# Kernel optimization log

Hardware: AMD Instinct MI355X
Metric: run time of the kernel (lower is better)

Reference implementation:

```python
import jax, jax.numpy as jnp
import numpy as np

RADIUS = 0.15
NSAMPLE = 128
NPOINT = 128
EPS = 1e-5  # BatchNorm eps (eval mode, running_mean=0, running_var=1)


def _bn(x, g, b):
    shape = (1, -1) + (1,) * (x.ndim - 2)
    return x * (g / jnp.sqrt(1.0 + EPS)).reshape(shape) + b.reshape(shape)


def _fps(x, npoint):
    # farthest point sampling; x: (Bk, N, 3) -> (Bk, npoint) int32
    Bn, N, _ = x.shape

    def step(carry, _):
        dist, far = carry
        c = jnp.take_along_axis(x, far[:, None, None], 1)  # (Bk,1,3)
        d = jnp.sum((x - c) ** 2, -1)
        dist = jnp.minimum(dist, d)
        return (dist, jnp.argmax(dist, -1).astype(jnp.int32)), far

    init = (jnp.full((Bn, N), 1e10, x.dtype), jnp.zeros((Bn,), jnp.int32))
    _, idxs = jax.lax.scan(step, init, None, length=npoint)
    return idxs.T  # (Bk, npoint)


def _sa_module(x, f, mlp):
    # PointnetSAModuleVotes: FPS -> ball query -> group (use_xyz, normalize_xyz)
    # -> shared MLP (conv2d 1x1 + BN + ReLU) -> max over nsample.
    Bk, M, _ = x.shape
    fps_idx = _fps(x, NPOINT)
    new_xyz = jnp.take_along_axis(x, fps_idx[..., None], 1)  # (Bk,np,3)
    d2 = jnp.sum((new_xyz[:, :, None, :] - x[:, None, :, :]) ** 2, -1)  # (Bk,np,M)
    cand = jnp.where(d2 < RADIUS ** 2, jnp.arange(M)[None, None, :], M)
    cand = jnp.sort(cand, -1)[..., :NSAMPLE]  # first nsample in-radius indices
    first = cand[..., :1]
    first = jnp.where(first == M, 0, first)
    idx = jnp.where(cand == M, first, cand)  # (Bk,np,ns), pad with first valid
    gx = jnp.take_along_axis(x, idx.reshape(Bk, -1)[..., None], 1).reshape(Bk, NPOINT, NSAMPLE, 3)
    gxn = (gx - new_xyz[:, :, None, :]) / RADIUS  # normalize_xyz=True
    gf = jnp.take_along_axis(f[:, :, None, :], idx[:, None, :, :], 3)  # (Bk,C,np,ns)
    h = jnp.concatenate([gxn.transpose(0, 3, 1, 2), gf], 1)  # (Bk, C+3, np, ns)
    for (w, b, g, be) in mlp:
        h = jax.nn.relu(_bn(jnp.einsum('oc,bcps->bops', w, h) + b[None, :, None, None], g, be))
    return new_xyz, h.max(-1)  # (Bk,np,3), (Bk,128,np)


def setup_inputs() -> dict:
    key = jax.random.key(0)
    ks = iter(jax.random.split(key, 40))
    B, M, K, C = 2, 1024, 19, 256
    inp = {}
    inp['xyz'] = jax.random.normal(next(ks), (B, M, K, 3), jnp.float32)
    inp['features'] = jax.random.normal(next(ks), (B, C, K, M), jnp.float32)

    def conv_p(prefix, cin, cout):
        inp[prefix + '_w'] = jax.random.normal(next(ks), (cout, cin), jnp.float32) * (1.0 / np.sqrt(cin))
        inp[prefix + '_b'] = jax.random.normal(next(ks), (cout,), jnp.float32) * 0.02
        inp[prefix + '_g'] = 1.0 + 0.1 * jax.random.normal(next(ks), (cout,), jnp.float32)
        inp[prefix + '_be'] = 0.02 * jax.random.normal(next(ks), (cout,), jnp.float32)

    conv_p('m1', C + 3, 128)  # use_xyz -> 259 in-channels
    conv_p('m2', 128, 128)
    conv_p('m3', 128, 128)
    conv_p('c1', 128, 128)
    conv_p('c2', 128, 128)
    inp['op_w'] = jax.random.normal(next(ks), (K, 5, 128), jnp.float32) * (1.0 / np.sqrt(128))
    inp['op_b'] = jax.random.normal(next(ks), (K, 5), jnp.float32) * 0.02
    return inp


def reference(xyz, features, m1_w, m1_b, m1_g, m1_be, m2_w, m2_b, m2_g, m2_be,
              m3_w, m3_b, m3_g, m3_be, c1_w, c1_b, c1_g, c1_be,
              c2_w, c2_b, c2_g, c2_be, op_w, op_b):
    B, M, K, _ = xyz.shape
    C = features.shape[1]
    # fold vote_factor k into the batch dim (all per-k SA/conv weights are shared)
    x = xyz.transpose(0, 2, 1, 3).reshape(B * K, M, 3)
    f = features.transpose(0, 2, 1, 3).reshape(B * K, C, M)
    mlp = [(m1_w, m1_b, m1_g, m1_be), (m2_w, m2_b, m2_g, m2_be), (m3_w, m3_b, m3_g, m3_be)]
    new_xyz, feat = _sa_module(x, f, mlp)
    net = jax.nn.relu(_bn(jnp.einsum('oc,bcp->bop', c1_w, feat) + c1_b[None, :, None], c1_g, c1_be))
    net = jax.nn.relu(_bn(jnp.einsum('oc,bcp->bop', c2_w, net) + c2_b[None, :, None], c2_g, c2_be))
    net = net.reshape(B, K, 128, NPOINT)
    # per-k output conv (conv_op ModuleList), 128 -> 2+3
    out = jnp.einsum('koc,bkcp->bkop', op_w, net) + op_b[None, :, :, None]
    net_t = out.transpose(0, 1, 3, 2)  # (B,K,np,5)
    agg_xyz = new_xyz.reshape(B, K, NPOINT, 3)
    center = agg_xyz + net_t[..., 2:5]  # decode_scores_
    scores = jnp.concatenate([net_t[..., :2], center], -1)  # obj(2) + center(3)
    return scores, agg_xyz, feat.reshape(B, K, 128, NPOINT)
```

## Files before the change

kernel.cpp:

```cpp
#include <hip/hip_runtime.h>
#include <math.h>

#define NBK   38

#define OFF_XC    0u
#define OFF_NXYZ  466944u
#define OFF_BIDX  525312u
#define OFF_W1F   3015680u
#define OFF_PREP  22938624u
#define OFF_WT    22955008u
#define OFF_WF    23086080u
#define OFF_CNT   23348224u

#define OUT_AGG   24320
#define OUT_FEAT  38912

typedef short bf16x8 __attribute__((ext_vector_type(8)));
typedef float f32x4  __attribute__((ext_vector_type(4)));
typedef int   v4i    __attribute__((ext_vector_type(4)));
typedef int   v2i    __attribute__((ext_vector_type(2)));

__device__ __forceinline__ float dist2f(float a0, float a1, float a2,
                                        float b0, float b1, float b2) {
#pragma clang fp contract(off)
  float d0 = a0 - b0;
  float d1 = a1 - b1;
  float d2 = a2 - b2;
  return d0 * d0 + d1 * d1 + d2 * d2;
}

__device__ __forceinline__ void split2rn(float v, unsigned& sh, unsigned& sm) {
  unsigned u = __float_as_uint(v);
  unsigned rh = (u + 0x7fffu + ((u >> 16) & 1u)) & 0xffff0000u;
  sh = rh >> 16;
  float r1 = v - __uint_as_float(rh);
  unsigned u1 = __float_as_uint(r1);
  unsigned rm = (u1 + 0x7fffu + ((u1 >> 16) & 1u)) & 0xffff0000u;
  sm = rm >> 16;
}

__global__ __launch_bounds__(256) void prep_kernel(
    const float* __restrict__ m1w, const float* __restrict__ m1g, const float* __restrict__ m1be,
    const float* __restrict__ m2b, const float* __restrict__ m2g, const float* __restrict__ m2be,
    const float* __restrict__ m3b, const float* __restrict__ m3g, const float* __restrict__ m3be,
    const float* __restrict__ c1b, const float* __restrict__ c1g, const float* __restrict__ c1be,
    const float* __restrict__ c2b, const float* __restrict__ c2g, const float* __restrict__ c2be,
    float* __restrict__ prep)
{
  int t = threadIdx.x;
  if (t < 128) {
    float inv = 1.0f / sqrtf(1.0f + 1e-5f);
    float a1 = m1g[t] * inv;
    prep[t] = a1;
    float a2 = m2g[t] * inv;  prep[256 + t] = a2;  prep[384 + t] = fmaf(m2b[t], a2, m2be[t]);
    float a3 = m3g[t] * inv;  prep[512 + t] = a3;  prep[640 + t] = fmaf(m3b[t], a3, m3be[t]);
    float ac1 = c1g[t] * inv; prep[768 + t] = ac1; prep[896 + t] = fmaf(c1b[t], ac1, c1be[t]);
    float ac2 = c2g[t] * inv; prep[1024 + t] = ac2; prep[1152 + t] = fmaf(c2b[t], ac2, c2be[t]);
    prep[1280 + 4 * t + 0] = m1w[t * 259 + 0] * a1;
    prep[1280 + 4 * t + 1] = m1w[t * 259 + 1] * a1;
    prep[1280 + 4 * t + 2] = m1w[t * 259 + 2] * a1;
    prep[1280 + 4 * t + 3] = m1be[t];
  }
}

__global__ __launch_bounds__(256) void wsplit_kernel(
    const float* __restrict__ m1w, const float* __restrict__ m2w,
    const float* __restrict__ m3w, const float* __restrict__ c1w,
    const float* __restrict__ c2w, short* __restrict__ Wf, float* __restrict__ wt)
{
  int idx = blockIdx.x * 256 + threadIdx.x;
#pragma unroll
  for (int e = 0; e < 4; ++e) {
    int i = idx * 4 + e;
    if (i < 32768) {
      int c = i & 127, o = (i >> 7) & 127, l = i >> 14;
      float w = (l ? m3w : m2w)[o * 128 + c];
      unsigned sh, sm;
      split2rn(w, sh, sm);
      int ot = o >> 4, mm = o & 15, kk = c >> 5, q = (c & 31) >> 3, j = c & 7;
      int within = (q * 16 + mm) * 8 + j;
      Wf[(((l * 2 + 0) * 4 + kk) * 8 + ot) * 512 + within] = (short)sh;
      Wf[(((l * 2 + 1) * 4 + kk) * 8 + ot) * 512 + within] = (short)sm;
    } else {
      int jdx = i - 32768;
      int o = jdx >> 8, c = jdx & 255;
      float w = m1w[o * 259 + 3 + c];
      unsigned sh, sm;
      split2rn(w, sh, sm);
      int ot = o >> 4, mm = o & 15, kk = c >> 5, q = (c & 31) >> 3, j = c & 7;
      int within = (q * 16 + mm) * 8 + j;
      Wf[65536 + ((kk) * 8 + ot) * 512 + within] = (short)sh;
      Wf[65536 + ((8 + kk) * 8 + ot) * 512 + within] = (short)sm;
    }
  }
  {
    int i = idx;
    int c = i >> 7, o = i & 127;
    wt[i] = c1w[o * 128 + c];
    wt[16384 + i] = c2w[o * 128 + c];
  }
}

__global__ __launch_bounds__(256) void fps_kernel(const float* __restrict__ xyz,
    float* __restrict__ xc, float* __restrict__ nxyz, float* __restrict__ agg)
{
  int bk = blockIdx.x, t = threadIdx.x;
  int b = bk / 19, k = bk % 19;
  int wave = t >> 6, lane = t & 63;
  __shared__ float sx0[1024], sx1[1024], sx2[1024];
  __shared__ unsigned long long skey[8];
  float x0[4], x1[4], x2[4], dist[4];
#pragma unroll
  for (int j = 0; j < 4; ++j) {
    int i = j * 256 + t;
    const float* src = xyz + ((size_t)((b * 1024 + i) * 19 + k)) * 3;
    x0[j] = src[0]; x1[j] = src[1]; x2[j] = src[2];
    sx0[i] = x0[j]; sx1[i] = x1[j]; sx2[i] = x2[j];
    xc[(bk * 3 + 0) * 1024 + i] = x0[j];
    xc[(bk * 3 + 1) * 1024 + i] = x1[j];
    xc[(bk * 3 + 2) * 1024 + i] = x2[j];
    dist[j] = 1e10f;
  }
  int far = 0;
  __syncthreads();
  for (int it = 0; it < 128; ++it) {
    float c0 = sx0[far], c1 = sx1[far], c2 = sx2[far];
    if (t < 3) {
      float cv = (t == 0) ? c0 : ((t == 1) ? c1 : c2);
      nxyz[(bk * 128 + it) * 3 + t] = cv;
      agg[(bk * 128 + it) * 3 + t]  = cv;
    }
    unsigned long long best = 0ull;
#pragma unroll
    for (int j = 0; j < 4; ++j) {
      int i = j * 256 + t;
      float d = dist2f(x0[j], x1[j], x2[j], c0, c1, c2);
      float dj = fminf(dist[j], d);
      dist[j] = dj;
      unsigned long long key =
          ((unsigned long long)__float_as_uint(dj) << 32) | (unsigned)(1023 - i);
      if (key > best) best = key;
    }
#pragma unroll
    for (int off = 32; off > 0; off >>= 1) {
      unsigned hi = (unsigned)(best >> 32), lo = (unsigned)best;
      unsigned h2 = __shfl_xor(hi, off);
      unsigned l2 = __shfl_xor(lo, off);
      unsigned long long ob = ((unsigned long long)h2 << 32) | l2;
      if (ob > best) best = ob;
    }
    if (lane == 0) skey[(it & 1) * 4 + wave] = best;
    __syncthreads();
    unsigned long long bb = skey[(it & 1) * 4 + (lane & 3)];
#pragma unroll
    for (int off = 1; off <= 2; off <<= 1) {
      unsigned hi = (unsigned)(bb >> 32), lo = (unsigned)bb;
      unsigned h2 = __shfl_xor(hi, off);
      unsigned l2 = __shfl_xor(lo, off);
      unsigned long long ob = ((unsigned long long)h2 << 32) | l2;
      if (ob > bb) bb = ob;
    }
    far = 1023 - (int)(bb & 0xffffffffu);
  }
}

__global__ __launch_bounds__(64) void ball_kernel(const float* __restrict__ xc,
    const float* __restrict__ nxyz, int* __restrict__ bidx, int* __restrict__ counts)
{
  int gb = blockIdx.x;
  int bk = gb >> 7, p = gb & 127, lane = threadIdx.x;
  const float* x0 = xc + (bk * 3 + 0) * 1024;
  const float* x1 = xc + (bk * 3 + 1) * 1024;
  const float* x2 = xc + (bk * 3 + 2) * 1024;
  float c0 = nxyz[(bk * 128 + p) * 3 + 0];
  float c1 = nxyz[(bk * 128 + p) * 3 + 1];
  float c2 = nxyz[(bk * 128 + p) * 3 + 2];
  int* out = bidx + ((size_t)gb) * 128;
  int count = 0, first = 0;
  bool got = false;
  for (int ch = 0; ch < 16 && count < 128; ++ch) {
    int m = (ch << 6) + lane;
    float d = dist2f(x0[m], x1[m], x2[m], c0, c1, c2);
    bool flag = d < 0.0225f;
    unsigned long long mask = __ballot(flag);
    if (!got && mask) { first = (ch << 6) + __builtin_ctzll(mask); got = true; }
    int pos = count + (int)__popcll(mask & ((1ull << lane) - 1ull));
    if (flag && pos < 128) out[pos] = m;
    count += (int)__popcll(mask);
  }
  for (int j = count + lane; j < 128; j += 64) out[j] = first;
  if (lane == 0) counts[gb] = count > 128 ? 128 : count;
}

__global__ __launch_bounds__(256, 2) void w1f_kernel(
    const float* __restrict__ feats, const float* __restrict__ m1b,
    const float* __restrict__ prep, const short* __restrict__ Wf,
    float* __restrict__ W1f)
{
  __shared__ __align__(16) short ffrag[16384];
  int blk = blockIdx.x;
  int bk = blk >> 3, m0 = (blk & 7) << 7;
  int b = bk / 19, k = bk % 19;
  int t = threadIdx.x;
  int wave = t >> 6, lane = t & 63;
  int quad = lane >> 4, nl = lane & 15;
  int mloc = t & 127, chalf = t >> 7;
  int st_w = mloc >> 4, sl_w = mloc & 15;
  const float* fbase = feats + ((size_t)(b * 4864 + k)) * 1024 + m0 + mloc;
  const short* WA = Wf + 65536;

  f32x4 acc[2][8];
#pragma unroll
  for (int oi = 0; oi < 2; ++oi)
#pragma unroll
    for (int st = 0; st < 8; ++st) acc[oi][st] = (f32x4){0.f, 0.f, 0.f, 0.f};

  for (int ch = 0; ch < 4; ++ch) {
    int cbase = ch * 64 + chalf * 32;
#pragma unroll
    for (int g = 0; g < 4; ++g) {
      float v[8];
#pragma unroll
      for (int j = 0; j < 8; ++j)
        v[j] = fbase[(size_t)(cbase + g * 8 + j) * 19456];
      unsigned sh[8], sm[8];
#pragma unroll
      for (int j = 0; j < 8; ++j) split2rn(v[j], sh[j], sm[j]);
      int base = chalf * 4096 + st_w * 512 + (g * 16 + sl_w) * 8;
      v4i ph = {(int)(sh[0] | (sh[1] << 16)), (int)(sh[2] | (sh[3] << 16)),
                (int)(sh[4] | (sh[5] << 16)), (int)(sh[6] | (sh[7] << 16))};
      *(v4i*)&ffrag[base] = ph;
      v4i pm = {(int)(sm[0] | (sm[1] << 16)), (int)(sm[2] | (sm[3] << 16)),
                (int)(sm[4] | (sm[5] << 16)), (int)(sm[6] | (sm[7] << 16))};
      *(v4i*)&ffrag[base + 8192] = pm;
    }
    __syncthreads();
#pragma unroll
    for (int kkl = 0; kkl < 2; ++kkl) {
      int kk = ch * 2 + kkl;
      bf16x8 a[2][2];
#pragma unroll
      for (int oi = 0; oi < 2; ++oi)
#pragma unroll
        for (int sp = 0; sp < 2; ++sp)
          a[oi][sp] = *(const bf16x8*)(WA + ((sp * 8 + kk) * 8 + wave * 2 + oi) * 512 + lane * 8);
#pragma unroll
      for (int st = 0; st < 8; ++st) {
        const short* hb = ffrag + kkl * 4096 + st * 512 + lane * 8;
        bf16x8 b0 = *(const bf16x8*)hb;
        bf16x8 b1 = *(const bf16x8*)(hb + 8192);
#pragma unroll
        for (int oi = 0; oi < 2; ++oi) {
          f32x4 c = acc[oi][st];
          c = __builtin_amdgcn_mfma_f32_16x16x32_bf16(a[oi][1], b0, c, 0, 0, 0);
          c = __builtin_amdgcn_mfma_f32_16x16x32_bf16(a[oi][0], b1, c, 0, 0, 0);
          c = __builtin_amdgcn_mfma_f32_16x16x32_bf16(a[oi][0], b0, c, 0, 0, 0);
          acc[oi][st] = c;
        }
      }
    }
    __syncthreads();
  }
#pragma unroll
  for (int oi = 0; oi < 2; ++oi) {
    int o0 = (wave * 2 + oi) * 16 + quad * 4;
    float4 bb = *(const float4*)&m1b[o0];
    float4 al = *(const float4*)&prep[o0];
#pragma unroll
    for (int st = 0; st < 8; ++st) {
      int m_out = m0 + st * 16 + nl;
      f32x4 cc = acc[oi][st];
      float4 r;
      r.x = (cc[0] + bb.x) * al.x;
      r.y = (cc[1] + bb.y) * al.y;
      r.z = (cc[2] + bb.z) * al.z;
      r.w = (cc[3] + bb.w) * al.w;
      *(float4*)&W1f[((size_t)(bk * 1024 + m_out)) * 128 + o0] = r;
    }
  }
}

__device__ __forceinline__ void mfma_layer(const short* __restrict__ Wf,
                                           const short* hfrag, int l,
                                           int wave, int lane, int nst_h,
                                           f32x4 acc[2][4])
{
#pragma unroll 1
  for (int kk = 0; kk < 4; ++kk) {
    bf16x8 a[2][2];
#pragma unroll
    for (int oi = 0; oi < 2; ++oi)
#pragma unroll
      for (int sp = 0; sp < 2; ++sp)
        a[oi][sp] = *(const bf16x8*)(Wf + (((l * 2 + sp) * 4 + kk) * 8 + (wave * 2 + oi)) * 512 + lane * 8);
    for (int st = 0; st < nst_h; ++st) {
      const short* hb = hfrag + kk * 2048 + st * 512 + lane * 8;
      bf16x8 b0 = *(const bf16x8*)(hb);
      bf16x8 b1 = *(const bf16x8*)(hb + 8192);
#pragma unroll
      for (int oi = 0; oi < 2; ++oi) {
        f32x4 c = acc[oi][st];
        c = __builtin_amdgcn_mfma_f32_16x16x32_bf16(a[oi][1], b0, c, 0, 0, 0);
        c = __builtin_amdgcn_mfma_f32_16x16x32_bf16(a[oi][0], b1, c, 0, 0, 0);
        c = __builtin_amdgcn_mfma_f32_16x16x32_bf16(a[oi][0], b0, c, 0, 0, 0);
        acc[oi][st] = c;
      }
    }
  }
}

__global__ __launch_bounds__(256, 4) void sa_kernel(
    const float* __restrict__ xc, const float* __restrict__ nxyz,
    const int* __restrict__ bidx, const int* __restrict__ counts,
    const float* __restrict__ W1f, const float* __restrict__ prep,
    const short* __restrict__ Wf, float* __restrict__ feat_out)
{
  __shared__ __align__(16) short hfrag[16384];
  __shared__ float pcs[512];
  int gb = blockIdx.x, bk = gb >> 7, p = gb & 127;
  int t = threadIdx.x;
  int wave = t >> 6, lane = t & 63;
  int quad = lane >> 4, nl = lane & 15;

  pcs[t] = prep[1280 + t];
  pcs[256 + t] = prep[1536 + t];

  int scount = counts[gb];
  int nst = (scount + 15) >> 4;

  float cen0 = nxyz[(bk * 128 + p) * 3 + 0];
  float cen1 = nxyz[(bk * 128 + p) * 3 + 1];
  float cen2 = nxyz[(bk * 128 + p) * 3 + 2];

  float rmax[2][4] = {{0.f, 0.f, 0.f, 0.f}, {0.f, 0.f, 0.f, 0.f}};
  __syncthreads();

  for (int hh = 0; hh < 2; ++hh) {
    int nst_h = nst - hh * 4;
    if (nst_h <= 0) break;
    if (nst_h > 4) nst_h = 4;
    {
      int cg = wave;
      int st = lane >> 4, sl = lane & 15;
      if (st < nst_h) {
        int m = bidx[((size_t)gb) * 128 + hh * 64 + lane];
        float g0 = (xc[(bk * 3 + 0) * 1024 + m] - cen0) * (1.0f / 0.15f);
        float g1 = (xc[(bk * 3 + 1) * 1024 + m] - cen1) * (1.0f / 0.15f);
        float g2 = (xc[(bk * 3 + 2) * 1024 + m] - cen2) * (1.0f / 0.15f);
        const float4* wrow = (const float4*)(W1f + ((size_t)(bk * 1024 + m)) * 128 + cg * 32);
        const float4* pcp = (const float4*)pcs + cg * 32;
#pragma unroll
        for (int g = 0; g < 4; ++g) {
          float4 wva = wrow[g * 2], wvb = wrow[g * 2 + 1];
          float wv[8] = {wva.x, wva.y, wva.z, wva.w, wvb.x, wvb.y, wvb.z, wvb.w};
          unsigned sh[8], sm[8];
#pragma unroll
          for (int e = 0; e < 8; ++e) {
            float4 pc = pcp[g * 8 + e];
            float hv = fmaxf(wv[e] + pc.x * g0 + pc.y * g1 + pc.z * g2 + pc.w, 0.f);
            split2rn(hv, sh[e], sm[e]);
          }
          int base = (cg * 4 + st) * 512 + (g * 16 + sl) * 8;
          v4i ph = {(int)(sh[0] | (sh[1] << 16)), (int)(sh[2] | (sh[3] << 16)),
                    (int)(sh[4] | (sh[5] << 16)), (int)(sh[6] | (sh[7] << 16))};
          *(v4i*)&hfrag[base] = ph;
          v4i pm = {(int)(sm[0] | (sm[1] << 16)), (int)(sm[2] | (sm[3] << 16)),
                    (int)(sm[4] | (sm[5] << 16)), (int)(sm[6] | (sm[7] << 16))};
          *(v4i*)&hfrag[base + 8192] = pm;
        }
      }
    }
    __syncthreads();

    f32x4 acc[2][4];
#pragma unroll
    for (int oi = 0; oi < 2; ++oi)
#pragma unroll
      for (int st = 0; st < 4; ++st) acc[oi][st] = (f32x4){0.f, 0.f, 0.f, 0.f};
    mfma_layer(Wf, hfrag, 0, wave, lane, nst_h, acc);
    __syncthreads();

#pragma unroll
    for (int oi = 0; oi < 2; ++oi) {
      int o0 = (wave * 2 + oi) * 16 + quad * 4;
      float4 al = *(const float4*)&prep[256 + o0];
      float4 be = *(const float4*)&prep[384 + o0];
      int kk2 = o0 >> 5, g2 = (o0 & 31) >> 3, j0 = o0 & 7;
      for (int st = 0; st < nst_h; ++st) {
        f32x4 cc = acc[oi][st];
        float v0 = fmaxf(fmaf(cc[0], al.x, be.x), 0.f);
        float v1 = fmaxf(fmaf(cc[1], al.y, be.y), 0.f);
        float v2 = fmaxf(fmaf(cc[2], al.z, be.z), 0.f);
        float v3 = fmaxf(fmaf(cc[3], al.w, be.w), 0.f);
        unsigned h0, m0_, h1, m1_, h2, m2_, h3, m3_;
        split2rn(v0, h0, m0_); split2rn(v1, h1, m1_);
        split2rn(v2, h2, m2_); split2rn(v3, h3, m3_);
        int base = (kk2 * 4 + st) * 512 + (g2 * 16 + nl) * 8 + j0;
        v2i w0 = {(int)(h0 | (h1 << 16)), (int)(h2 | (h3 << 16))};
        *(v2i*)&hfrag[base] = w0;
        v2i w1 = {(int)(m0_ | (m1_ << 16)), (int)(m2_ | (m3_ << 16))};
        *(v2i*)&hfrag[base + 8192] = w1;
      }
    }
    __syncthreads();

#pragma unroll
    for (int oi = 0; oi < 2; ++oi)
#pragma unroll
      for (int st = 0; st < 4; ++st) acc[oi][st] = (f32x4){0.f, 0.f, 0.f, 0.f};
    mfma_layer(Wf, hfrag, 1, wave, lane, nst_h, acc);

#pragma unroll
    for (int oi = 0; oi < 2; ++oi) {
      int o0 = (wave * 2 + oi) * 16 + quad * 4;
      float4 al = *(const float4*)&prep[512 + o0];
      float4 be = *(const float4*)&prep[640 + o0];
      for (int st = 0; st < nst_h; ++st) {
        f32x4 cc = acc[oi][st];
        rmax[oi][0] = fmaxf(rmax[oi][0], fmaxf(fmaf(cc[0], al.x, be.x), 0.f));
        rmax[oi][1] = fmaxf(rmax[oi][1], fmaxf(fmaf(cc[1], al.y, be.y), 0.f));
        rmax[oi][2] = fmaxf(rmax[oi][2], fmaxf(fmaf(cc[2], al.z, be.z), 0.f));
        rmax[oi][3] = fmaxf(rmax[oi][3], fmaxf(fmaf(cc[3], al.w, be.w), 0.f));
      }
    }
    __syncthreads();
  }

#pragma unroll
  for (int oi = 0; oi < 2; ++oi)
#pragma unroll
    for (int r = 0; r < 4; ++r) {
      float v = rmax[oi][r];
      v = fmaxf(v, __shfl_xor(v, 1));
      v = fmaxf(v, __shfl_xor(v, 2));
      v = fmaxf(v, __shfl_xor(v, 4));
      v = fmaxf(v, __shfl_xor(v, 8));
      if (nl == 0) {
        int o = (wave * 2 + oi) * 16 + quad * 4 + r;
        feat_out[(((size_t)bk) << 14) + (o << 7) + p] = v;
      }
    }
}

__device__ __forceinline__ void gemm_tile(const float* __restrict__ w,
                                          const float* lds, int tx, int ty,
                                          float acc[8][8])
{
#pragma unroll
  for (int i = 0; i < 8; ++i)
#pragma unroll
    for (int j = 0; j < 8; ++j) acc[i][j] = 0.f;
  for (int c = 0; c < 128; ++c) {
    const float4* wr = (const float4*)(w + c * 128 + ty * 8);
    float4 a0 = wr[0], a1 = wr[1];
    const float4* hr = (const float4*)(lds + c * 128 + tx * 8);
    float4 b0 = hr[0], b1 = hr[1];
    float av[8] = {a0.x, a0.y, a0.z, a0.w, a1.x, a1.y, a1.z, a1.w};
    float bv[8] = {b0.x, b0.y, b0.z, b0.w, b1.x, b1.y, b1.z, b1.w};
#pragma unroll
    for (int i = 0; i < 8; ++i)
#pragma unroll
      for (int j = 0; j < 8; ++j) acc[i][j] = fmaf(av[i], bv[j], acc[i][j]);
  }
}

__global__ __launch_bounds__(256) void head_kernel(const float* __restrict__ featg,
    const float* __restrict__ prep, const float* __restrict__ wt,
    const float* __restrict__ nxyz, const float* __restrict__ opw,
    const float* __restrict__ opb, float* __restrict__ scores)
{
  __shared__ __align__(16) float buf[128 * 128];
  int bk = blockIdx.x, t = threadIdx.x;
  for (int i = t; i < 16384; i += 256) buf[i] = featg[(bk << 14) + i];
  __syncthreads();
  int tx = t & 15, ty = t >> 4;
  float acc[8][8];

  gemm_tile(wt, buf, tx, ty, acc);
  __syncthreads();
#pragma unroll
  for (int i = 0; i < 8; ++i) {
    int o = ty * 8 + i;
    float al = prep[768 + o], be = prep[896 + o];
#pragma unroll
    for (int j = 0; j < 8; ++j)
      buf[o * 128 + tx * 8 + j] = fmaxf(fmaf(acc[i][j], al, be), 0.f);
  }
  __syncthreads();

  gemm_tile(wt + 16384, buf, tx, ty, acc);
  __syncthreads();
#pragma unroll
  for (int i = 0; i < 8; ++i) {
    int o = ty * 8 + i;
    float al = prep[1024 + o], be = prep[1152 + o];
#pragma unroll
    for (int j = 0; j < 8; ++j)
      buf[o * 128 + tx * 8 + j] = fmaxf(fmaf(acc[i][j], al, be), 0.f);
  }
  __syncthreads();

  if (t < 128) {
    int p = t, k = bk % 19;
    float res[5];
#pragma unroll
    for (int j = 0; j < 5; ++j) {
      const float* wr = opw + ((size_t)(k * 5 + j)) * 128;
      float a = opb[k * 5 + j];
      for (int c = 0; c < 128; ++c) a = fmaf(wr[c], buf[c * 128 + p], a);
      res[j] = a;
    }
    float a0 = nxyz[(bk * 128 + p) * 3 + 0];
    float a1 = nxyz[(bk * 128 + p) * 3 + 1];
    float a2 = nxyz[(bk * 128 + p) * 3 + 2];
    float* sc = scores + ((size_t)(bk * 128 + p)) * 5;
    sc[0] = res[0];
    sc[1] = res[1];
    sc[2] = a0 + res[2];
    sc[3] = a1 + res[3];
    sc[4] = a2 + res[4];
  }
}

extern "C" void kernel_launch(void* const* d_in, const int* in_sizes, int n_in,
                              void* d_out, int out_size, void* d_ws, size_t ws_size,
                              hipStream_t stream) {
  (void)in_sizes; (void)n_in; (void)out_size; (void)ws_size;
  const float* xyz  = (const float*)d_in[0];
  const float* fts  = (const float*)d_in[1];
  const float* m1w  = (const float*)d_in[2];
  const float* m1b  = (const float*)d_in[3];
  const float* m1g  = (const float*)d_in[4];
  const float* m1be = (const float*)d_in[5];
  const float* m2w  = (const float*)d_in[6];
  const float* m2b  = (const float*)d_in[7];
  const float* m2g  = (const float*)d_in[8];
  const float* m2be = (const float*)d_in[9];
  const float* m3w  = (const float*)d_in[10];
  const float* m3b  = (const float*)d_in[11];
  const float* m3g  = (const float*)d_in[12];
  const float* m3be = (const float*)d_in[13];
  const float* c1w  = (const float*)d_in[14];
  const float* c1b  = (const float*)d_in[15];
  const float* c1g  = (const float*)d_in[16];
  const float* c1be = (const float*)d_in[17];
  const float* c2w  = (const float*)d_in[18];
  const float* c2b  = (const float*)d_in[19];
  const float* c2g  = (const float*)d_in[20];
  const float* c2be = (const float*)d_in[21];
  const float* opw  = (const float*)d_in[22];
  const float* opb  = (const float*)d_in[23];

  float* out = (float*)d_out;
  char* ws = (char*)d_ws;
  float* xc   = (float*)(ws + OFF_XC);
  float* nxyz = (float*)(ws + OFF_NXYZ);
  int*   bidx = (int*)(ws + OFF_BIDX);
  float* W1f  = (float*)(ws + OFF_W1F);
  float* prep = (float*)(ws + OFF_PREP);
  float* wt   = (float*)(ws + OFF_WT);
  short* Wf   = (short*)(ws + OFF_WF);
  int*   cnt  = (int*)(ws + OFF_CNT);

  hipLaunchKernelGGL(prep_kernel, dim3(1), dim3(256), 0, stream,
                     m1w, m1g, m1be, m2b, m2g, m2be, m3b, m3g, m3be,
                     c1b, c1g, c1be, c2b, c2g, c2be, prep);
  hipLaunchKernelGGL(wsplit_kernel, dim3(64), dim3(256), 0, stream,
                     m1w, m2w, m3w, c1w, c2w, Wf, wt);
  hipLaunchKernelGGL(fps_kernel, dim3(NBK), dim3(256), 0, stream,
                     xyz, xc, nxyz, out + OUT_AGG);
  hipLaunchKernelGGL(ball_kernel, dim3(NBK * 128), dim3(64), 0, stream,
                     xc, nxyz, bidx, cnt);
  hipLaunchKernelGGL(w1f_kernel, dim3(NBK * 8), dim3(256), 0, stream,
                     fts, m1b, prep, Wf, W1f);
  hipLaunchKernelGGL(sa_kernel, dim3(NBK * 128), dim3(256), 0, stream,
                     xc, nxyz, bidx, cnt, W1f, prep, Wf, out + OUT_FEAT);
  hipLaunchKernelGGL(head_kernel, dim3(NBK), dim3(256), 0, stream,
                     out + OUT_FEAT, prep, wt, nxyz, opw, opb, out);
}
```

Measured before the change: 342.3 us.

## Pack four centroids' sample tiles per SA block and simplify FPS argmax

The SA kernel now processes four sampled centroids per block. It concatenates their 16-sample tiles into a shared stream, so partially filled tiles no longer waste MFMA work and block count drops fourfold. Per-tile max results go to shared memory and are reduced per centroid at the end. FPS replaces the 64-bit key shuffle reduction with a float max reduction plus ballot, and carries the winner's coordinates through shared memory instead of indexing a shared point copy. The costs are extra shared memory, a lower occupancy hint, and fewer blocks, which may underfill the GPU.

```diff
diff --git a/kernel.cpp b/kernel.cpp
--- a/kernel.cpp
+++ b/kernel.cpp
@@ -107,60 +107,82 @@
   int bk = blockIdx.x, t = threadIdx.x;
   int b = bk / 19, k = bk % 19;
   int wave = t >> 6, lane = t & 63;
-  __shared__ float sx0[1024], sx1[1024], sx2[1024];
-  __shared__ unsigned long long skey[8];
+  __shared__ int scand[2][4][8];
   float x0[4], x1[4], x2[4], dist[4];
 #pragma unroll
   for (int j = 0; j < 4; ++j) {
     int i = j * 256 + t;
     const float* src = xyz + ((size_t)((b * 1024 + i) * 19 + k)) * 3;
     x0[j] = src[0]; x1[j] = src[1]; x2[j] = src[2];
-    sx0[i] = x0[j]; sx1[i] = x1[j]; sx2[i] = x2[j];
     xc[(bk * 3 + 0) * 1024 + i] = x0[j];
     xc[(bk * 3 + 1) * 1024 + i] = x1[j];
     xc[(bk * 3 + 2) * 1024 + i] = x2[j];
     dist[j] = 1e10f;
   }
-  int far = 0;
-  __syncthreads();
+  if (t == 0) {
+#pragma unroll
+    for (int w = 0; w < 4; ++w) {
+      scand[0][w][0] = 0;
+      scand[0][w][1] = 1023;
+      scand[0][w][2] = __float_as_int(x0[0]);
+      scand[0][w][3] = __float_as_int(x1[0]);
+      scand[0][w][4] = __float_as_int(x2[0]);
+    }
+  }
+  __syncthreads();
+
   for (int it = 0; it < 128; ++it) {
-    float c0 = sx0[far], c1 = sx1[far], c2 = sx2[far];
+    int pi = it & 1;
+    v4i s0 = *(const v4i*)&scand[pi][0][0]; int z0 = scand[pi][0][4];
+    v4i s1 = *(const v4i*)&scand[pi][1][0]; int z1 = scand[pi][1][4];
+    v4i s2 = *(const v4i*)&scand[pi][2][0]; int z2 = scand[pi][2][4];
+    v4i s3 = *(const v4i*)&scand[pi][3][0]; int z3 = scand[pi][3][4];
+    unsigned long long k0 = ((unsigned long long)(unsigned)s0.x << 32) | (unsigned)s0.y;
+    unsigned long long k1 = ((unsigned long long)(unsigned)s1.x << 32) | (unsigned)s1.y;
+    unsigned long long k2 = ((unsigned long long)(unsigned)s2.x << 32) | (unsigned)s2.y;
+    unsigned long long k3 = ((unsigned long long)(unsigned)s3.x << 32) | (unsigned)s3.y;
+    if (k1 > k0) { k0 = k1; s0 = s1; z0 = z1; }
+    if (k3 > k2) { k2 = k3; s2 = s3; z2 = z3; }
+    if (k2 > k0) { k0 = k2; s0 = s2; z0 = z2; }
+    float c0 = __int_as_float(s0.z);
+    float c1 = __int_as_float(s0.w);
+    float c2 = __int_as_float(z0);
     if (t < 3) {
       float cv = (t == 0) ? c0 : ((t == 1) ? c1 : c2);
       nxyz[(bk * 128 + it) * 3 + t] = cv;
       agg[(bk * 128 + it) * 3 + t]  = cv;
     }
-    unsigned long long best = 0ull;
 #pragma unroll
     for (int j = 0; j < 4; ++j) {
-      int i = j * 256 + t;
       float d = dist2f(x0[j], x1[j], x2[j], c0, c1, c2);
-      float dj = fminf(dist[j], d);
-      dist[j] = dj;
-      unsigned long long key =
-          ((unsigned long long)__float_as_uint(dj) << 32) | (unsigned)(1023 - i);
-      if (key > best) best = key;
-    }
-#pragma unroll
-    for (int off = 32; off > 0; off >>= 1) {
-      unsigned hi = (unsigned)(best >> 32), lo = (unsigned)best;
-      unsigned h2 = __shfl_xor(hi, off);
-      unsigned l2 = __shfl_xor(lo, off);
-      unsigned long long ob = ((unsigned long long)h2 << 32) | l2;
-      if (ob > best) best = ob;
-    }
-    if (lane == 0) skey[(it & 1) * 4 + wave] = best;
+      dist[j] = fminf(dist[j], d);
+    }
+    float dmax = fmaxf(fmaxf(dist[0], dist[1]), fmaxf(dist[2], dist[3]));
+#pragma unroll
+    for (int off = 1; off <= 32; off <<= 1)
+      dmax = fmaxf(dmax, __shfl_xor(dmax, off));
+    unsigned long long b0 = __ballot(dist[0] == dmax);
+    unsigned long long b1 = __ballot(dist[1] == dmax);
+    unsigned long long b2 = __ballot(dist[2] == dmax);
+    unsigned long long b3 = __ballot(dist[3] == dmax);
+    int idx;
+    if (b0)      idx =       (wave << 6) + __builtin_ctzll(b0);
+    else if (b1) idx = 256 + (wave << 6) + __builtin_ctzll(b1);
+    else if (b2) idx = 512 + (wave << 6) + __builtin_ctzll(b2);
+    else         idx = 768 + (wave << 6) + __builtin_ctzll(b3);
+    if (lane == (idx & 63)) {
+      int j = idx >> 8;
+      float w0 = (j == 0) ? x0[0] : (j == 1) ? x0[1] : (j == 2) ? x0[2] : x0[3];
+      float w1 = (j == 0) ? x1[0] : (j == 1) ? x1[1] : (j == 2) ? x1[2] : x1[3];
+      float w2 = (j == 0) ? x2[0] : (j == 1) ? x2[1] : (j == 2) ? x2[2] : x2[3];
+      int* slot = &scand[pi ^ 1][wave][0];
+      slot[0] = __float_as_int(dmax);
+      slot[1] = 1023 - idx;
+      slot[2] = __float_as_int(w0);
+      slot[3] = __float_as_int(w1);
+      slot[4] = __float_as_int(w2);
+    }
     __syncthreads();
-    unsigned long long bb = skey[(it & 1) * 4 + (lane & 3)];
-#pragma unroll
-    for (int off = 1; off <= 2; off <<= 1) {
-      unsigned hi = (unsigned)(bb >> 32), lo = (unsigned)bb;
-      unsigned h2 = __shfl_xor(hi, off);
-      unsigned l2 = __shfl_xor(lo, off);
-      unsigned long long ob = ((unsigned long long)h2 << 32) | l2;
-      if (ob > bb) bb = ob;
-    }
-    far = 1023 - (int)(bb & 0xffffffffu);
   }
 }
 
@@ -309,7 +331,7 @@
   }
 }
 
-__global__ __launch_bounds__(256, 4) void sa_kernel(
+__global__ __launch_bounds__(256, 3) void sa_kernel(
     const float* __restrict__ xc, const float* __restrict__ nxyz,
     const int* __restrict__ bidx, const int* __restrict__ counts,
     const float* __restrict__ W1f, const float* __restrict__ prep,
@@ -317,33 +339,41 @@
 {
   __shared__ __align__(16) short hfrag[16384];
   __shared__ float pcs[512];
-  int gb = blockIdx.x, bk = gb >> 7, p = gb & 127;
+  __shared__ float sm[32 * 128];
+  __shared__ float ccen[12];
+  __shared__ int scnt[4];
+  int gb = blockIdx.x, bk = gb >> 5, pb = (gb & 31) << 2;
   int t = threadIdx.x;
   int wave = t >> 6, lane = t & 63;
   int quad = lane >> 4, nl = lane & 15;
 
   pcs[t] = prep[1280 + t];
   pcs[256 + t] = prep[1536 + t];
-
-  int scount = counts[gb];
-  int nst = (scount + 15) >> 4;
-
-  float cen0 = nxyz[(bk * 128 + p) * 3 + 0];
-  float cen1 = nxyz[(bk * 128 + p) * 3 + 1];
-  float cen2 = nxyz[(bk * 128 + p) * 3 + 2];
-
-  float rmax[2][4] = {{0.f, 0.f, 0.f, 0.f}, {0.f, 0.f, 0.f, 0.f}};
-  __syncthreads();
-
-  for (int hh = 0; hh < 2; ++hh) {
-    int nst_h = nst - hh * 4;
-    if (nst_h <= 0) break;
+  if (t < 4) scnt[t] = counts[bk * 128 + pb + t];
+  if (t < 12) ccen[t] = nxyz[(bk * 128 + pb + (t >> 2) % 4) * 3 + 0];
+  __syncthreads();
+  if (t < 12) {
+    int bb = t / 3, c = t % 3;
+    ccen[t] = nxyz[(bk * 128 + pb + bb) * 3 + c];
+  }
+  int n0 = (scnt[0] + 15) >> 4, n1 = (scnt[1] + 15) >> 4;
+  int n2 = (scnt[2] + 15) >> 4, n3 = (scnt[3] + 15) >> 4;
+  int pf1 = n0, pf2 = n0 + n1, pf3 = n0 + n1 + n2, T = n0 + n1 + n2 + n3;
+  __syncthreads();
+
+  for (int q0 = 0; q0 < T; q0 += 4) {
+    int nst_h = T - q0;
     if (nst_h > 4) nst_h = 4;
     {
       int cg = wave;
       int st = lane >> 4, sl = lane & 15;
       if (st < nst_h) {
-        int m = bidx[((size_t)gb) * 128 + hh * 64 + lane];
+        int q = q0 + st;
+        int bq = (q >= pf1) + (q >= pf2) + (q >= pf3);
+        int tstart = (bq == 0) ? 0 : (bq == 1) ? pf1 : (bq == 2) ? pf2 : pf3;
+        int tslot = q - tstart;
+        int m = bidx[((size_t)(bk * 128 + pb + bq)) * 128 + tslot * 16 + sl];
+        float cen0 = ccen[bq * 3 + 0], cen1 = ccen[bq * 3 + 1], cen2 = ccen[bq * 3 + 2];
         float g0 = (xc[(bk * 3 + 0) * 1024 + m] - cen0) * (1.0f / 0.15f);
         float g1 = (xc[(bk * 3 + 1) * 1024 + m] - cen1) * (1.0f / 0.15f);
         float g2 = (xc[(bk * 3 + 2) * 1024 + m] - cen2) * (1.0f / 0.15f);
@@ -353,19 +383,19 @@
         for (int g = 0; g < 4; ++g) {
           float4 wva = wrow[g * 2], wvb = wrow[g * 2 + 1];
           float wv[8] = {wva.x, wva.y, wva.z, wva.w, wvb.x, wvb.y, wvb.z, wvb.w};
-          unsigned sh[8], sm[8];
+          unsigned sh[8], smv[8];
 #pragma unroll
           for (int e = 0; e < 8; ++e) {
             float4 pc = pcp[g * 8 + e];
             float hv = fmaxf(wv[e] + pc.x * g0 + pc.y * g1 + pc.z * g2 + pc.w, 0.f);
-            split2rn(hv, sh[e], sm[e]);
+            split2rn(hv, sh[e], smv[e]);
           }
           int base = (cg * 4 + st) * 512 + (g * 16 + sl) * 8;
           v4i ph = {(int)(sh[0] | (sh[1] << 16)), (int)(sh[2] | (sh[3] << 16)),
                     (int)(sh[4] | (sh[5] << 16)), (int)(sh[6] | (sh[7] << 16))};
           *(v4i*)&hfrag[base] = ph;
-          v4i pm = {(int)(sm[0] | (sm[1] << 16)), (int)(sm[2] | (sm[3] << 16)),
-                    (int)(sm[4] | (sm[5] << 16)), (int)(sm[6] | (sm[7] << 16))};
+          v4i pm = {(int)(smv[0] | (smv[1] << 16)), (int)(smv[2] | (smv[3] << 16)),
+                    (int)(smv[4] | (smv[5] << 16)), (int)(smv[6] | (smv[7] << 16))};
           *(v4i*)&hfrag[base + 8192] = pm;
         }
       }
@@ -417,29 +447,34 @@
       float4 be = *(const float4*)&prep[640 + o0];
       for (int st = 0; st < nst_h; ++st) {
         f32x4 cc = acc[oi][st];
-        rmax[oi][0] = fmaxf(rmax[oi][0], fmaxf(fmaf(cc[0], al.x, be.x), 0.f));
-        rmax[oi][1] = fmaxf(rmax[oi][1], fmaxf(fmaf(cc[1], al.y, be.y), 0.f));
-        rmax[oi][2] = fmaxf(rmax[oi][2], fmaxf(fmaf(cc[2], al.z, be.z), 0.f));
-        rmax[oi][3] = fmaxf(rmax[oi][3], fmaxf(fmaf(cc[3], al.w, be.w), 0.f));
+        float v[4];
+        v[0] = fmaxf(fmaf(cc[0], al.x, be.x), 0.f);
+        v[1] = fmaxf(fmaf(cc[1], al.y, be.y), 0.f);
+        v[2] = fmaxf(fmaf(cc[2], al.z, be.z), 0.f);
+        v[3] = fmaxf(fmaf(cc[3], al.w, be.w), 0.f);
+#pragma unroll
+        for (int r = 0; r < 4; ++r) {
+          float x = v[r];
+          x = fmaxf(x, __shfl_xor(x, 1));
+          x = fmaxf(x, __shfl_xor(x, 2));
+          x = fmaxf(x, __shfl_xor(x, 4));
+          x = fmaxf(x, __shfl_xor(x, 8));
+          if (nl == 0) sm[(q0 + st) * 128 + o0 + r] = x;
+        }
       }
     }
     __syncthreads();
   }
 
 #pragma unroll
-  for (int oi = 0; oi < 2; ++oi)
-#pragma unroll
-    for (int r = 0; r < 4; ++r) {
-      float v = rmax[oi][r];
-      v = fmaxf(v, __shfl_xor(v, 1));
-      v = fmaxf(v, __shfl_xor(v, 2));
-      v = fmaxf(v, __shfl_xor(v, 4));
-      v = fmaxf(v, __shfl_xor(v, 8));
-      if (nl == 0) {
-        int o = (wave * 2 + oi) * 16 + quad * 4 + r;
-        feat_out[(((size_t)bk) << 14) + (o << 7) + p] = v;
-      }
-    }
+  for (int e = t; e < 512; e += 256) {
+    int bb = e >> 7, o = e & 127;
+    int qs = (bb == 0) ? 0 : (bb == 1) ? pf1 : (bb == 2) ? pf2 : pf3;
+    int nq = (bb == 0) ? n0 : (bb == 1) ? n1 : (bb == 2) ? n2 : n3;
+    float v = sm[qs * 128 + o];
+    for (int q = 1; q < nq; ++q) v = fmaxf(v, sm[(qs + q) * 128 + o]);
+    feat_out[(((size_t)bk) << 14) + (o << 7) + pb + bb] = v;
+  }
 }
 
 __device__ __forceinline__ void gemm_tile(const float* __restrict__ w,
@@ -573,7 +608,7 @@
                      xc, nxyz, bidx, cnt);
   hipLaunchKernelGGL(w1f_kernel, dim3(NBK * 8), dim3(256), 0, stream,
                      fts, m1b, prep, Wf, W1f);
-  hipLaunchKernelGGL(sa_kernel, dim3(NBK * 128), dim3(256), 0, stream,
+  hipLaunchKernelGGL(sa_kernel, dim3(NBK * 32), dim3(256), 0, stream,
                      xc, nxyz, bidx, cnt, W1f, prep, Wf, out + OUT_FEAT);
   hipLaunchKernelGGL(head_kernel, dim3(NBK), dim3(256), 0, stream,
                      out + OUT_FEAT, prep, wt, nxyz, opw, opb, out);
```

Measured after the change: 356.5 us. 4.1% more time.
